# Kernel tuning notes

Measured on AMD Instinct MI355X. Metric: run time of the kernel, lower is better.

Reference implementation:

```python
import jax, jax.numpy as jnp
import numpy as np
from jax import lax

N, DIM, K, B = 400000, 128, 27, 8


def setup_inputs() -> dict:
    key = jax.random.key(0)
    ks = jax.random.split(key, 8)
    feats = jax.random.normal(ks[0], (N, DIM), dtype=jnp.float32)
    neighbor_idx = jax.random.randint(ks[1], (N, K), 0, N, dtype=jnp.int32)
    neighbor_mask = jax.random.randint(ks[2], (N, K), 0, 2) > 0
    segment_ids = jnp.sort(jax.random.randint(ks[3], (N,), 0, B, dtype=jnp.int32))
    s = 1.0 / np.sqrt(DIM)
    W1 = jax.random.normal(ks[4], (K, DIM, DIM), dtype=jnp.float32) * s
    W2 = jax.random.normal(ks[5], (K, DIM, DIM), dtype=jnp.float32) * s
    W3 = jax.random.normal(ks[6], (DIM, DIM), dtype=jnp.float32) * s
    b1 = jnp.zeros((DIM,), jnp.float32)
    b2 = jnp.zeros((DIM,), jnp.float32)
    b3 = jnp.zeros((DIM,), jnp.float32)
    return {"feats": feats, "neighbor_idx": neighbor_idx, "neighbor_mask": neighbor_mask,
            "segment_ids": segment_ids, "num_segments": B,
            "W1": W1, "b1": b1, "W2": W2, "b2": b2, "W3": W3, "b3": b3}


def sparse_conv3(x, idx, mask, W, b):
    # x: [N,D]; idx/mask: [N,K]; W: [K,D,D] -> y[n] = sum_k mask[n,k] * x[idx[n,k]] @ W[k] + b
    def step(acc, kin):
        ik, mk, Wk = kin  # [N], [N], [D,D]
        g = jnp.where(mk[:, None], x[ik], 0.0)  # [N,D] gather per offset
        return acc + g @ Wk, None
    acc, _ = lax.scan(step, jnp.zeros_like(x), (idx.T, mask.T, W))
    return acc + b


def reference(feats, neighbor_idx, neighbor_mask, segment_ids, num_segments,
              W1, b1, W2, b2, W3, b3):
    out1 = jax.nn.relu(sparse_conv3(feats, neighbor_idx, neighbor_mask, W1, b1))
    out2 = jax.nn.relu(sparse_conv3(feats, neighbor_idx, neighbor_mask, W2, b2))
    # per-batch: outer(mean over channels of out1 [Ni,1], mean over points of out2 [1,D])
    sums = jax.ops.segment_sum(out2, segment_ids, num_segments=num_segments)  # [B,D]
    cnts = jax.ops.segment_sum(jnp.ones((out2.shape[0],), out2.dtype), segment_ids,
                               num_segments=num_segments)  # [B]
    seg_mean2 = sums / jnp.maximum(cnts, 1.0)[:, None]  # [B,D]
    row_mean1 = jnp.mean(out1, axis=-1, keepdims=True)  # [N,1]
    enc = jnp.sqrt(row_mean1 * seg_mean2[segment_ids] + 1e-12)  # [N,D]
    mid = enc + out1 + out2
    out3 = jax.nn.relu(mid @ W3 + b3)  # kernel_size=1 conv == pointwise linear
    return jax.nn.relu(feats - out3)
```

## Files before the change

### kernel.cpp

```cpp
#include <hip/hip_runtime.h>
#include <stdint.h>

#define NPTS 400000
#define DIM  128
#define KNB  27
#define NSEG 8

typedef _Float16 f16x8 __attribute__((ext_vector_type(8)));
typedef float floatx16 __attribute__((ext_vector_type(16)));

#define OFF_FEATSH 0UL
#define OFF_OUT1   102400000UL
#define OFF_OUT2   204800000UL
#define OFF_PW1    307200000UL
#define OFF_PW2    308084736UL
#define OFF_PW3    308969472UL
#define OFF_SEG    309002240UL
#define OFF_CNT    309006336UL
#define OFF_ZROW   309006368UL
#define ZOFF       309006368

#define LDS_A_OFF  131072

__device__ __forceinline__ void load_lds16(const void* g, void* l) {
  __builtin_amdgcn_global_load_lds(
      (const __attribute__((address_space(1))) void*)g,
      (__attribute__((address_space(3))) void*)l, 16, 0, 0);
}

__global__ __launch_bounds__(256) void cvt_feats(const float* __restrict__ f,
                                                 _Float16* __restrict__ fh) {
  size_t g = (size_t)blockIdx.x * 256 + threadIdx.x;
  const float4* src = (const float4*)f;
  float4 v0 = src[g * 2], v1 = src[g * 2 + 1];
  f16x8 o;
  o[0] = (_Float16)v0.x; o[1] = (_Float16)v0.y; o[2] = (_Float16)v0.z; o[3] = (_Float16)v0.w;
  o[4] = (_Float16)v1.x; o[5] = (_Float16)v1.y; o[6] = (_Float16)v1.z; o[7] = (_Float16)v1.w;
  ((f16x8*)fh)[g] = o;
}

__global__ __launch_bounds__(256) void pack_w(const float* __restrict__ W1,
                                              const float* __restrict__ W2,
                                              const float* __restrict__ W3,
                                              _Float16* __restrict__ pW1,
                                              _Float16* __restrict__ pW2,
                                              _Float16* __restrict__ pW3) {
  int gid = blockIdx.x * 256 + threadIdx.x;
  const float* W; _Float16* dst; int k, rem;
  if (gid < 110592) {
    int mat = gid / 55296, r = gid % 55296;
    W = mat ? W2 : W1; dst = (mat ? pW2 : pW1) + (size_t)r * 8;
    k = r >> 11; rem = r & 2047;
  } else {
    int r = gid - 110592;
    W = W3; dst = pW3 + (size_t)r * 8; k = 0; rem = r;
  }
  int ko = rem >> 8, ct = (rem >> 6) & 3, lane = rem & 63;
  int h = lane >> 5, c = ct * 32 + (lane & 31);
  f16x8 o;
#pragma unroll
  for (int j = 0; j < 8; ++j) {
    int kk = ko * 16 + h * 8 + j;
    o[j] = (_Float16)W[(size_t)(k * 128 + kk) * 128 + c];
  }
  *(f16x8*)dst = o;
}

__global__ __launch_bounds__(512, 2) void conv_kernel(
    const _Float16* __restrict__ featsh, const int* __restrict__ nidx,
    const int* __restrict__ nmask, const int* __restrict__ segids,
    const _Float16* __restrict__ pW1, const _Float16* __restrict__ pW2,
    const float* __restrict__ b1, const float* __restrict__ b2,
    _Float16* __restrict__ out1, _Float16* __restrict__ out2,
    float* __restrict__ seg_sums, float* __restrict__ cnts_f) {
  __shared__ __align__(16) char lds_raw[163840];
  int tid = threadIdx.x, ws = tid >> 6, lane = tid & 63, h = lane >> 5;
  int conv = ws >> 2, g2 = ws & 3;
  int n0 = blockIdx.x * 128;
  int srow = ws * 16 + (lane >> 2);
  int jlane = lane & 3;
  size_t gidx = (size_t)(n0 + srow) * KNB;

  const char* fb = (const char*)featsh;
  const char* srcW = (const char*)(ws < 4 ? pW1 : pW2) + (size_t)(ws & 3) * 8192;

  floatx16 acc[4];
#pragma unroll
  for (int ct = 0; ct < 4; ++ct)
#pragma unroll
    for (int r = 0; r < 16; ++r) acc[ct][r] = 0.f;

  int i_nxt, m_nxt;
  {
    int i0 = nidx[gidx + 0];
    int m0 = nmask[gidx + 0];
    i_nxt = nidx[gidx + 1];
    m_nxt = nmask[gidx + 1];
    int off = m0 ? i0 * 256 : ZOFF;
    uint4 ag[4];
#pragma unroll
    for (int j = 0; j < 4; ++j)
      ag[j] = *(const uint4*)(fb + off + j * 64 + jlane * 16);
#pragma unroll
    for (int it = 0; it < 8; ++it)
      load_lds16(srcW + it * 1024 + lane * 16, lds_raw + ws * 8192 + it * 1024);
#pragma unroll
    for (int j = 0; j < 4; ++j)
      *(uint4*)(lds_raw + LDS_A_OFF + (size_t)(j * 4 + jlane) * 2048 + srow * 16) = ag[j];
    asm volatile("s_waitcnt lgkmcnt(0)" ::: "memory");
  }

  for (int k = 0; k < KNB; ++k) {
    int off = m_nxt ? i_nxt * 256 : ZOFF;
    uint4 ag[4];
#pragma unroll
    for (int j = 0; j < 4; ++j)
      ag[j] = *(const uint4*)(fb + off + j * 64 + jlane * 16);
    __builtin_amdgcn_sched_barrier(0);
    {
      int kq = (k + 2 <= KNB - 1) ? k + 2 : KNB - 1;
      i_nxt = nidx[gidx + kq];
      m_nxt = nmask[gidx + kq];
    }
    __builtin_amdgcn_sched_barrier(0);
    {
      int ks = (k + 1 <= KNB - 1) ? k + 1 : KNB - 1;
      const char* sk = srcW + (size_t)ks * 32768;
      char* db = lds_raw + ((k + 1) & 1) * 65536 + ws * 8192;
#pragma unroll
      for (int it = 0; it < 8; ++it)
        load_lds16(sk + it * 1024 + lane * 16, db + it * 1024);
    }
    __builtin_amdgcn_sched_barrier(0);
    asm volatile("s_waitcnt vmcnt(14)" ::: "memory");
    __builtin_amdgcn_s_barrier();
    __builtin_amdgcn_sched_barrier(0);

    const char* ldsA = lds_raw + LDS_A_OFF;
    const _Float16* ldsW =
        (const _Float16*)(lds_raw + (k & 1) * 65536 + conv * 32768);
#pragma unroll
    for (int ko = 0; ko < 8; ++ko) {
      f16x8 a = *(const f16x8*)(ldsA + (size_t)(ko * 2 + h) * 2048 +
                                (g2 * 32 + (lane & 31)) * 16);
#pragma unroll
      for (int ct = 0; ct < 4; ++ct) {
        f16x8 b = *(const f16x8*)(ldsW + ((ko * 4 + ct) * 64 + lane) * 8);
        acc[ct] = __builtin_amdgcn_mfma_f32_32x32x16_f16(a, b, acc[ct], 0, 0, 0);
      }
    }
    __builtin_amdgcn_sched_barrier(0);
    __builtin_amdgcn_s_barrier();
    __builtin_amdgcn_sched_barrier(0);
#pragma unroll
    for (int j = 0; j < 4; ++j)
      *(uint4*)(lds_raw + LDS_A_OFF + (size_t)(j * 4 + jlane) * 2048 + srow * 16) = ag[j];
    asm volatile("s_waitcnt lgkmcnt(0)" ::: "memory");
    __builtin_amdgcn_sched_barrier(0);
  }

  const float* bb = conv ? b2 : b1;
  float bias[4];
#pragma unroll
  for (int ct = 0; ct < 4; ++ct) bias[ct] = bb[ct * 32 + (lane & 31)];
#pragma unroll
  for (int ct = 0; ct < 4; ++ct)
#pragma unroll
    for (int r = 0; r < 16; ++r)
      acc[ct][r] = fmaxf(acc[ct][r] + bias[ct], 0.f);

  int seg0 = segids[n0];
  bool uniform = (seg0 == segids[n0 + 127]);

  if (conv == 1 && uniform) {
#pragma unroll
    for (int ct = 0; ct < 4; ++ct) {
      float s = 0.f;
#pragma unroll
      for (int r = 0; r < 16; ++r) s += acc[ct][r];
      s += __shfl_xor(s, 32);
      if (lane < 32) atomicAdd(&seg_sums[seg0 * 128 + ct * 32 + lane], s);
    }
  }
  if (tid == 0 && uniform) atomicAdd(&cnts_f[seg0], 128.0f);

  __syncthreads();
  _Float16* lds_out = (_Float16*)lds_raw;
#pragma unroll
  for (int ct = 0; ct < 4; ++ct) {
    int col = ct * 32 + (lane & 31);
#pragma unroll
    for (int r = 0; r < 16; ++r) {
      int lr = g2 * 32 + (r & 3) + 8 * (r >> 2) + 4 * h;
      lds_out[conv * 16384 + lr * 128 + col] = (_Float16)acc[ct][r];
    }
  }
  __syncthreads();

  if (!uniform && tid < 128) {
    int s = segids[n0 + tid];
    atomicAdd(&cnts_f[s], 1.0f);
    for (int c = 0; c < 128; ++c)
      atomicAdd(&seg_sums[s * 128 + c], (float)lds_out[16384 + tid * 128 + c]);
  }

#pragma unroll
  for (int it = 0; it < 8; ++it) {
    int chunk = it * 512 + tid;
    int cv = chunk >> 11;
    int off16 = chunk & 2047;
    uint4 v = *(const uint4*)(lds_raw + cv * 32768 + off16 * 16);
    *(uint4*)((cv ? out2 : out1) + (size_t)n0 * 128 + off16 * 8) = v;
  }
}

__global__ __launch_bounds__(256, 2) void final_kernel(
    const float* __restrict__ feats, const _Float16* __restrict__ out1,
    const _Float16* __restrict__ out2, const int* __restrict__ segids,
    const float* __restrict__ seg_sums, const float* __restrict__ cnts_f,
    const char* __restrict__ pW3, const float* __restrict__ b3,
    float* __restrict__ dout) {
  __shared__ __align__(16) char ldsw3[32768];
  __shared__ float smean[NSEG * 128];
  int tid = threadIdx.x, w = tid >> 6, lane = tid & 63, h = lane >> 5;
  int n0 = blockIdx.x * 128;
#pragma unroll
  for (int it = 0; it < 8; ++it)
    load_lds16(pW3 + w * 8192 + it * 1024 + lane * 16, ldsw3 + w * 8192 + it * 1024);
  for (int i = tid; i < NSEG * 128; i += 256)
    smean[i] = seg_sums[i] / fmaxf(cnts_f[i >> 7], 1.0f);
  __syncthreads();

  int row = n0 + w * 32 + (lane & 31);
  int seg = segids[row];
  const char* p1 = (const char*)(out1 + (size_t)row * 128 + h * 8);
  const char* p2 = (const char*)(out2 + (size_t)row * 128 + h * 8);
  f16x8 o1[8], o2[8];
  float s1 = 0.f;
#pragma unroll
  for (int ko = 0; ko < 8; ++ko) {
    o1[ko] = *(const f16x8*)(p1 + ko * 32);
    o2[ko] = *(const f16x8*)(p2 + ko * 32);
#pragma unroll
    for (int j = 0; j < 8; ++j) s1 += (float)o1[ko][j];
  }
  s1 += __shfl_xor(s1, 32);
  float rm = s1 * (1.0f / 128.0f);

  f16x8 a[8];
#pragma unroll
  for (int ko = 0; ko < 8; ++ko) {
    int colb = ko * 16 + h * 8;
#pragma unroll
    for (int j = 0; j < 8; ++j) {
      float m2 = smean[seg * 128 + colb + j];
      float e = sqrtf(fmaf(rm, m2, 1e-12f));
      a[ko][j] = (_Float16)(e + (float)o1[ko][j] + (float)o2[ko][j]);
    }
  }
  floatx16 acc[4];
#pragma unroll
  for (int ct = 0; ct < 4; ++ct)
#pragma unroll
    for (int r = 0; r < 16; ++r) acc[ct][r] = 0.f;
#pragma unroll
  for (int ko = 0; ko < 8; ++ko)
#pragma unroll
    for (int ct = 0; ct < 4; ++ct) {
      f16x8 b = *(const f16x8*)(ldsw3 + ((ko * 4 + ct) * 64 + lane) * 16);
      acc[ct] = __builtin_amdgcn_mfma_f32_32x32x16_f16(a[ko], b, acc[ct], 0, 0, 0);
    }
#pragma unroll
  for (int ct = 0; ct < 4; ++ct) {
    int col = ct * 32 + (lane & 31);
    float bc = b3[col];
#pragma unroll
    for (int r = 0; r < 16; ++r) {
      int gr = n0 + w * 32 + (r & 3) + 8 * (r >> 2) + 4 * h;
      float v = fmaxf(acc[ct][r] + bc, 0.f);
      float f = feats[(size_t)gr * 128 + col];
      dout[(size_t)gr * 128 + col] = fmaxf(f - v, 0.f);
    }
  }
}

extern "C" void kernel_launch(void* const* d_in, const int* in_sizes, int n_in,
                              void* d_out, int out_size, void* d_ws, size_t ws_size,
                              hipStream_t stream) {
  (void)in_sizes; (void)n_in; (void)out_size; (void)ws_size;
  const float* feats = (const float*)d_in[0];
  const int* nidx   = (const int*)d_in[1];
  const int* nmask  = (const int*)d_in[2];
  const int* segids = (const int*)d_in[3];
  const float* W1 = (const float*)d_in[5];
  const float* b1 = (const float*)d_in[6];
  const float* W2 = (const float*)d_in[7];
  const float* b2 = (const float*)d_in[8];
  const float* W3 = (const float*)d_in[9];
  const float* b3 = (const float*)d_in[10];
  float* dout = (float*)d_out;
  char* ws = (char*)d_ws;

  _Float16* featsh = (_Float16*)(ws + OFF_FEATSH);
  _Float16* out1h  = (_Float16*)(ws + OFF_OUT1);
  _Float16* out2h  = (_Float16*)(ws + OFF_OUT2);
  _Float16* pW1    = (_Float16*)(ws + OFF_PW1);
  _Float16* pW2    = (_Float16*)(ws + OFF_PW2);
  _Float16* pW3    = (_Float16*)(ws + OFF_PW3);
  float* seg_sums  = (float*)(ws + OFF_SEG);
  float* cnts_f    = (float*)(ws + OFF_CNT);

  hipMemsetAsync(ws + OFF_SEG, 0, 4096 + 32 + 256, stream);
  cvt_feats<<<25000, 256, 0, stream>>>(feats, featsh);
  pack_w<<<440, 256, 0, stream>>>(W1, W2, W3, pW1, pW2, pW3);
  conv_kernel<<<3125, 512, 0, stream>>>(featsh, nidx, nmask, segids, pW1, pW2,
                                        b1, b2, out1h, out2h, seg_sums, cnts_f);
  final_kernel<<<3125, 256, 0, stream>>>(feats, out1h, out2h, segids, seg_sums,
                                         cnts_f, (const char*)pW3, b3, dout);
}
```

Baseline: 1.570 ms.

## Double conv tile to 256 rows, single-buffer weights, swizzle gathered LDS

The conv kernel now handles 256 points per block instead of 128. Each wave computes two 32-row MFMA tiles that share each weight fragment read from LDS, which halves how often each weight slice is reloaded per point. Weights are now single-buffered, and the gathered feature tile is stored with an XOR swizzle to avoid bank conflicts. This frees LDS for the larger A tile, but the weight load can no longer overlap the MFMA work and now needs a full vmcnt(0) wait and barrier on every k step. A tail-block guard is added because the point count does not divide evenly by 256, and register pressure rises with the two accumulator sets.

```diff
diff --git a/kernel.cpp b/kernel.cpp
--- a/kernel.cpp
+++ b/kernel.cpp
@@ -20,7 +20,7 @@
 #define OFF_ZROW   309006368UL
 #define ZOFF       309006368
 
-#define LDS_A_OFF  131072
+#define LDS_W_OFF  65536
 
 __device__ __forceinline__ void load_lds16(const void* g, void* l) {
   __builtin_amdgcn_global_load_lds(
@@ -73,89 +73,109 @@
     const float* __restrict__ b1, const float* __restrict__ b2,
     _Float16* __restrict__ out1, _Float16* __restrict__ out2,
     float* __restrict__ seg_sums, float* __restrict__ cnts_f) {
-  __shared__ __align__(16) char lds_raw[163840];
+  __shared__ __align__(16) char lds_raw[131072];
   int tid = threadIdx.x, ws = tid >> 6, lane = tid & 63, h = lane >> 5;
-  int conv = ws >> 2, g2 = ws & 3;
-  int n0 = blockIdx.x * 128;
-  int srow = ws * 16 + (lane >> 2);
+  int conv = ws >> 2;
+  int n0 = blockIdx.x * 256;
   int jlane = lane & 3;
-  size_t gidx = (size_t)(n0 + srow) * KNB;
+  int srowA = ws * 32 + (lane >> 2);
+  int srowB = srowA + 16;
+  int growA = n0 + srowA, growB = n0 + srowB;
+  bool vA = growA < NPTS, vB = growB < NPTS;
+  size_t gxA = (size_t)(vA ? growA : NPTS - 1) * KNB;
+  size_t gxB = (size_t)(vB ? growB : NPTS - 1) * KNB;
+  int r0 = (ws & 3) * 64 + (lane & 31);
+  int r1 = r0 + 32;
 
   const char* fb = (const char*)featsh;
   const char* srcW = (const char*)(ws < 4 ? pW1 : pW2) + (size_t)(ws & 3) * 8192;
-
-  floatx16 acc[4];
+  char* wdst = lds_raw + LDS_W_OFF + (conv ? 32768 : 0) + (ws & 3) * 8192;
+
+  floatx16 acc0[4], acc1[4];
 #pragma unroll
   for (int ct = 0; ct < 4; ++ct)
 #pragma unroll
-    for (int r = 0; r < 16; ++r) acc[ct][r] = 0.f;
-
-  int i_nxt, m_nxt;
+    for (int r = 0; r < 16; ++r) { acc0[ct][r] = 0.f; acc1[ct][r] = 0.f; }
+
+  uint4 agA[4], agB[4];
+  int iN_A, mN_A, iN_B, mN_B;
+
   {
-    int i0 = nidx[gidx + 0];
-    int m0 = nmask[gidx + 0];
-    i_nxt = nidx[gidx + 1];
-    m_nxt = nmask[gidx + 1];
-    int off = m0 ? i0 * 256 : ZOFF;
-    uint4 ag[4];
-#pragma unroll
-    for (int j = 0; j < 4; ++j)
-      ag[j] = *(const uint4*)(fb + off + j * 64 + jlane * 16);
+    int iA = nidx[gxA], mA = vA ? nmask[gxA] : 0;
+    int iB = nidx[gxB], mB = vB ? nmask[gxB] : 0;
+    int offA = mA ? iA * 256 : ZOFF;
+    int offB = mB ? iB * 256 : ZOFF;
+#pragma unroll
+    for (int q = 0; q < 4; ++q) {
+      agA[q] = *(const uint4*)(fb + offA + q * 64 + jlane * 16);
+      agB[q] = *(const uint4*)(fb + offB + q * 64 + jlane * 16);
+    }
 #pragma unroll
     for (int it = 0; it < 8; ++it)
-      load_lds16(srcW + it * 1024 + lane * 16, lds_raw + ws * 8192 + it * 1024);
-#pragma unroll
-    for (int j = 0; j < 4; ++j)
-      *(uint4*)(lds_raw + LDS_A_OFF + (size_t)(j * 4 + jlane) * 2048 + srow * 16) = ag[j];
-    asm volatile("s_waitcnt lgkmcnt(0)" ::: "memory");
+      load_lds16(srcW + it * 1024 + lane * 16, wdst + it * 1024);
+    iN_A = nidx[gxA + 1]; mN_A = vA ? nmask[gxA + 1] : 0;
+    iN_B = nidx[gxB + 1]; mN_B = vB ? nmask[gxB + 1] : 0;
+#pragma unroll
+    for (int q = 0; q < 4; ++q) {
+      int cA = q * 4 + jlane;
+      *(uint4*)(lds_raw + cA * 4096 + (srowA ^ cA) * 16) = agA[q];
+      *(uint4*)(lds_raw + cA * 4096 + (srowB ^ cA) * 16) = agB[q];
+    }
+    __syncthreads();
   }
 
   for (int k = 0; k < KNB; ++k) {
-    int off = m_nxt ? i_nxt * 256 : ZOFF;
-    uint4 ag[4];
-#pragma unroll
-    for (int j = 0; j < 4; ++j)
-      ag[j] = *(const uint4*)(fb + off + j * 64 + jlane * 16);
+    int offA = mN_A ? iN_A * 256 : ZOFF;
+    int offB = mN_B ? iN_B * 256 : ZOFF;
+    __builtin_amdgcn_sched_barrier(0);
+#pragma unroll
+    for (int q = 0; q < 4; ++q) {
+      agA[q] = *(const uint4*)(fb + offA + q * 64 + jlane * 16);
+      agB[q] = *(const uint4*)(fb + offB + q * 64 + jlane * 16);
+    }
     __builtin_amdgcn_sched_barrier(0);
     {
       int kq = (k + 2 <= KNB - 1) ? k + 2 : KNB - 1;
-      i_nxt = nidx[gidx + kq];
-      m_nxt = nmask[gidx + kq];
-    }
-    __builtin_amdgcn_sched_barrier(0);
+      iN_A = nidx[gxA + kq]; mN_A = vA ? nmask[gxA + kq] : 0;
+      iN_B = nidx[gxB + kq]; mN_B = vB ? nmask[gxB + kq] : 0;
+    }
+    __builtin_amdgcn_sched_barrier(0);
+
+    const _Float16* ldsW = (const _Float16*)(lds_raw + LDS_W_OFF + conv * 32768);
+#pragma unroll
+    for (int ko = 0; ko < 8; ++ko) {
+      int c0 = ko * 2 + h;
+      f16x8 a0 = *(const f16x8*)(lds_raw + c0 * 4096 + (r0 ^ c0) * 16);
+      f16x8 a1 = *(const f16x8*)(lds_raw + c0 * 4096 + (r1 ^ c0) * 16);
+#pragma unroll
+      for (int ct = 0; ct < 4; ++ct) {
+        f16x8 b = *(const f16x8*)(ldsW + ((ko * 4 + ct) * 64 + lane) * 8);
+        acc0[ct] = __builtin_amdgcn_mfma_f32_32x32x16_f16(a0, b, acc0[ct], 0, 0, 0);
+        acc1[ct] = __builtin_amdgcn_mfma_f32_32x32x16_f16(a1, b, acc1[ct], 0, 0, 0);
+      }
+    }
+    __builtin_amdgcn_sched_barrier(0);
+    __builtin_amdgcn_s_barrier();
+    __builtin_amdgcn_sched_barrier(0);
+
+#pragma unroll
+    for (int q = 0; q < 4; ++q) {
+      int cA = q * 4 + jlane;
+      *(uint4*)(lds_raw + cA * 4096 + (srowA ^ cA) * 16) = agA[q];
+      *(uint4*)(lds_raw + cA * 4096 + (srowB ^ cA) * 16) = agB[q];
+    }
     {
       int ks = (k + 1 <= KNB - 1) ? k + 1 : KNB - 1;
       const char* sk = srcW + (size_t)ks * 32768;
-      char* db = lds_raw + ((k + 1) & 1) * 65536 + ws * 8192;
 #pragma unroll
       for (int it = 0; it < 8; ++it)
-        load_lds16(sk + it * 1024 + lane * 16, db + it * 1024);
-    }
-    __builtin_amdgcn_sched_barrier(0);
-    asm volatile("s_waitcnt vmcnt(14)" ::: "memory");
+        load_lds16(sk + it * 1024 + lane * 16, wdst + it * 1024);
+    }
+    __builtin_amdgcn_sched_barrier(0);
+    asm volatile("s_waitcnt lgkmcnt(0)" ::: "memory");
+    asm volatile("s_waitcnt vmcnt(0)" ::: "memory");
+    __builtin_amdgcn_sched_barrier(0);
     __builtin_amdgcn_s_barrier();
-    __builtin_amdgcn_sched_barrier(0);
-
-    const char* ldsA = lds_raw + LDS_A_OFF;
-    const _Float16* ldsW =
-        (const _Float16*)(lds_raw + (k & 1) * 65536 + conv * 32768);
-#pragma unroll
-    for (int ko = 0; ko < 8; ++ko) {
-      f16x8 a = *(const f16x8*)(ldsA + (size_t)(ko * 2 + h) * 2048 +
-                                (g2 * 32 + (lane & 31)) * 16);
-#pragma unroll
-      for (int ct = 0; ct < 4; ++ct) {
-        f16x8 b = *(const f16x8*)(ldsW + ((ko * 4 + ct) * 64 + lane) * 8);
-        acc[ct] = __builtin_amdgcn_mfma_f32_32x32x16_f16(a, b, acc[ct], 0, 0, 0);
-      }
-    }
-    __builtin_amdgcn_sched_barrier(0);
-    __builtin_amdgcn_s_barrier();
-    __builtin_amdgcn_sched_barrier(0);
-#pragma unroll
-    for (int j = 0; j < 4; ++j)
-      *(uint4*)(lds_raw + LDS_A_OFF + (size_t)(j * 4 + jlane) * 2048 + srow * 16) = ag[j];
-    asm volatile("s_waitcnt lgkmcnt(0)" ::: "memory");
     __builtin_amdgcn_sched_barrier(0);
   }
 
@@ -166,23 +186,26 @@
 #pragma unroll
   for (int ct = 0; ct < 4; ++ct)
 #pragma unroll
-    for (int r = 0; r < 16; ++r)
-      acc[ct][r] = fmaxf(acc[ct][r] + bias[ct], 0.f);
-
+    for (int r = 0; r < 16; ++r) {
+      acc0[ct][r] = fmaxf(acc0[ct][r] + bias[ct], 0.f);
+      acc1[ct][r] = fmaxf(acc1[ct][r] + bias[ct], 0.f);
+    }
+
+  int nvalid = (NPTS - n0 < 256) ? (NPTS - n0) : 256;
   int seg0 = segids[n0];
-  bool uniform = (seg0 == segids[n0 + 127]);
+  bool uniform = (nvalid == 256) && (seg0 == segids[n0 + 255]);
 
   if (conv == 1 && uniform) {
 #pragma unroll
     for (int ct = 0; ct < 4; ++ct) {
       float s = 0.f;
 #pragma unroll
-      for (int r = 0; r < 16; ++r) s += acc[ct][r];
+      for (int r = 0; r < 16; ++r) s += acc0[ct][r] + acc1[ct][r];
       s += __shfl_xor(s, 32);
       if (lane < 32) atomicAdd(&seg_sums[seg0 * 128 + ct * 32 + lane], s);
     }
   }
-  if (tid == 0 && uniform) atomicAdd(&cnts_f[seg0], 128.0f);
+  if (tid == 0 && uniform) atomicAdd(&cnts_f[seg0], 256.0f);
 
   __syncthreads();
   _Float16* lds_out = (_Float16*)lds_raw;
@@ -191,26 +214,31 @@
     int col = ct * 32 + (lane & 31);
 #pragma unroll
     for (int r = 0; r < 16; ++r) {
-      int lr = g2 * 32 + (r & 3) + 8 * (r >> 2) + 4 * h;
-      lds_out[conv * 16384 + lr * 128 + col] = (_Float16)acc[ct][r];
+      int lr = (ws & 3) * 64 + (r & 3) + 8 * (r >> 2) + 4 * h;
+      lds_out[conv * 32768 + lr * 128 + col] = (_Float16)acc0[ct][r];
+      lds_out[conv * 32768 + (lr + 32) * 128 + col] = (_Float16)acc1[ct][r];
     }
   }
   __syncthreads();
 
-  if (!uniform && tid < 128) {
-    int s = segids[n0 + tid];
-    atomicAdd(&cnts_f[s], 1.0f);
-    for (int c = 0; c < 128; ++c)
-      atomicAdd(&seg_sums[s * 128 + c], (float)lds_out[16384 + tid * 128 + c]);
-  }
-
-#pragma unroll
-  for (int it = 0; it < 8; ++it) {
+  if (!uniform && tid < 256) {
+    if (n0 + tid < NPTS) {
+      int s = segids[n0 + tid];
+      atomicAdd(&cnts_f[s], 1.0f);
+      for (int c = 0; c < 128; ++c)
+        atomicAdd(&seg_sums[s * 128 + c], (float)lds_out[32768 + tid * 128 + c]);
+    }
+  }
+
+#pragma unroll
+  for (int it = 0; it < 16; ++it) {
     int chunk = it * 512 + tid;
-    int cv = chunk >> 11;
-    int off16 = chunk & 2047;
-    uint4 v = *(const uint4*)(lds_raw + cv * 32768 + off16 * 16);
-    *(uint4*)((cv ? out2 : out1) + (size_t)n0 * 128 + off16 * 8) = v;
+    int cv = chunk >> 12;
+    int off16 = chunk & 4095;
+    if (n0 + (off16 >> 4) < NPTS) {
+      uint4 v = *(const uint4*)(lds_raw + cv * 65536 + off16 * 16);
+      *(uint4*)((cv ? out2 : out1) + (size_t)n0 * 128 + (size_t)off16 * 8) = v;
+    }
   }
 }
 
@@ -313,7 +341,7 @@
   hipMemsetAsync(ws + OFF_SEG, 0, 4096 + 32 + 256, stream);
   cvt_feats<<<25000, 256, 0, stream>>>(feats, featsh);
   pack_w<<<440, 256, 0, stream>>>(W1, W2, W3, pW1, pW2, pW3);
-  conv_kernel<<<3125, 512, 0, stream>>>(featsh, nidx, nmask, segids, pW1, pW2,
+  conv_kernel<<<1563, 512, 0, stream>>>(featsh, nidx, nmask, segids, pW1, pW2,
                                         b1, b2, out1h, out2h, seg_sums, cnts_f);
   final_kernel<<<3125, 256, 0, stream>>>(feats, out1h, out2h, segids, seg_sums,
                                          cnts_f, (const char*)pW3, b3, dout);
```

Result: slower. 1.864 ms (+18.7%).

## Split K across warp pairs with 64-row tiles, swizzled A in LDS, and LDS reduction

Applied to the files above, without the earlier changes.

Re-partitions the MFMA work so each warp computes a 64-row tile (two 32-row accumulators sharing each B fragment) over half of the K dimension. The partial sums from the two warp halves are reduced through LDS scratch before bias and ReLU. The gather tile in LDS gets an XOR swizzle to avoid bank conflicts, and the gather loads are reordered to issue after the weight prefetch, with a single barrier-free wait. This doubles B-fragment reuse and accumulator registers and adds an LDS reduction step in the epilogue.

```diff
diff --git a/kernel.cpp b/kernel.cpp
--- a/kernel.cpp
+++ b/kernel.cpp
@@ -20,7 +20,8 @@
 #define OFF_ZROW   309006368UL
 #define ZOFF       309006368
 
-#define LDS_A_OFF  131072
+#define LDSA       0
+#define LDSW       32768
 
 __device__ __forceinline__ void load_lds16(const void* g, void* l) {
   __builtin_amdgcn_global_load_lds(
@@ -75,109 +76,144 @@
     float* __restrict__ seg_sums, float* __restrict__ cnts_f) {
   __shared__ __align__(16) char lds_raw[163840];
   int tid = threadIdx.x, ws = tid >> 6, lane = tid & 63, h = lane >> 5;
-  int conv = ws >> 2, g2 = ws & 3;
+  int c_ = ws >> 2, g = (ws >> 1) & 1, j = ws & 1;
   int n0 = blockIdx.x * 128;
-  int srow = ws * 16 + (lane >> 2);
-  int jlane = lane & 3;
-  size_t gidx = (size_t)(n0 + srow) * KNB;
+  int srow = tid >> 2, jl = tid & 3;
+  size_t gx = (size_t)(n0 + srow) * KNB;
+  int r0 = g * 64 + (lane & 31), r1 = r0 + 32;
 
   const char* fb = (const char*)featsh;
   const char* srcW = (const char*)(ws < 4 ? pW1 : pW2) + (size_t)(ws & 3) * 8192;
 
-  floatx16 acc[4];
+  floatx16 acc0[4], acc1[4];
 #pragma unroll
   for (int ct = 0; ct < 4; ++ct)
 #pragma unroll
-    for (int r = 0; r < 16; ++r) acc[ct][r] = 0.f;
-
-  int i_nxt, m_nxt;
+    for (int r = 0; r < 16; ++r) { acc0[ct][r] = 0.f; acc1[ct][r] = 0.f; }
+
+  uint4 ag[4];
+  int i_n, m_n;
+
   {
-    int i0 = nidx[gidx + 0];
-    int m0 = nmask[gidx + 0];
-    i_nxt = nidx[gidx + 1];
-    m_nxt = nmask[gidx + 1];
+    int i0 = nidx[gx], m0 = nmask[gx];
     int off = m0 ? i0 * 256 : ZOFF;
-    uint4 ag[4];
-#pragma unroll
-    for (int j = 0; j < 4; ++j)
-      ag[j] = *(const uint4*)(fb + off + j * 64 + jlane * 16);
+#pragma unroll
+    for (int q = 0; q < 4; ++q)
+      ag[q] = *(const uint4*)(fb + off + (q * 4 + jl) * 16);
 #pragma unroll
     for (int it = 0; it < 8; ++it)
-      load_lds16(srcW + it * 1024 + lane * 16, lds_raw + ws * 8192 + it * 1024);
-#pragma unroll
-    for (int j = 0; j < 4; ++j)
-      *(uint4*)(lds_raw + LDS_A_OFF + (size_t)(j * 4 + jlane) * 2048 + srow * 16) = ag[j];
-    asm volatile("s_waitcnt lgkmcnt(0)" ::: "memory");
+      load_lds16(srcW + it * 1024 + lane * 16, lds_raw + LDSW + ws * 8192 + it * 1024);
+    i_n = nidx[gx + 1]; m_n = nmask[gx + 1];
+#pragma unroll
+    for (int q = 0; q < 4; ++q) {
+      int cA = q * 4 + jl;
+      *(uint4*)(lds_raw + cA * 2048 + ((srow ^ (2 * cA)) << 4)) = ag[q];
+    }
+    __syncthreads();
   }
 
   for (int k = 0; k < KNB; ++k) {
-    int off = m_nxt ? i_nxt * 256 : ZOFF;
-    uint4 ag[4];
-#pragma unroll
-    for (int j = 0; j < 4; ++j)
-      ag[j] = *(const uint4*)(fb + off + j * 64 + jlane * 16);
-    __builtin_amdgcn_sched_barrier(0);
-    {
-      int kq = (k + 2 <= KNB - 1) ? k + 2 : KNB - 1;
-      i_nxt = nidx[gidx + kq];
-      m_nxt = nmask[gidx + kq];
-    }
-    __builtin_amdgcn_sched_barrier(0);
     {
       int ks = (k + 1 <= KNB - 1) ? k + 1 : KNB - 1;
       const char* sk = srcW + (size_t)ks * 32768;
-      char* db = lds_raw + ((k + 1) & 1) * 65536 + ws * 8192;
+      char* db = lds_raw + LDSW + ((k + 1) & 1) * 65536 + ws * 8192;
 #pragma unroll
       for (int it = 0; it < 8; ++it)
         load_lds16(sk + it * 1024 + lane * 16, db + it * 1024);
     }
     __builtin_amdgcn_sched_barrier(0);
-    asm volatile("s_waitcnt vmcnt(14)" ::: "memory");
+    {
+      int off = m_n ? i_n * 256 : ZOFF;
+#pragma unroll
+      for (int q = 0; q < 4; ++q)
+        ag[q] = *(const uint4*)(fb + off + (q * 4 + jl) * 16);
+    }
+    __builtin_amdgcn_sched_barrier(0);
+    {
+      int kq2 = (k + 2 <= KNB - 1) ? k + 2 : KNB - 1;
+      i_n = nidx[gx + kq2]; m_n = nmask[gx + kq2];
+    }
+    __builtin_amdgcn_sched_barrier(0);
+    {
+      const char* wb = lds_raw + LDSW + (k & 1) * 65536 + c_ * 32768;
+#pragma unroll
+      for (int kq = 0; kq < 4; ++kq) {
+        int ko = j * 4 + kq;
+        int c0 = ko * 2 + h;
+        f16x8 a0 = *(const f16x8*)(lds_raw + c0 * 2048 + ((r0 ^ (2 * c0)) << 4));
+        f16x8 a1 = *(const f16x8*)(lds_raw + c0 * 2048 + ((r1 ^ (2 * c0)) << 4));
+#pragma unroll
+        for (int ct = 0; ct < 4; ++ct) {
+          f16x8 b = *(const f16x8*)(wb + ((ko * 4 + ct) * 64 + lane) * 16);
+          acc0[ct] = __builtin_amdgcn_mfma_f32_32x32x16_f16(a0, b, acc0[ct], 0, 0, 0);
+          acc1[ct] = __builtin_amdgcn_mfma_f32_32x32x16_f16(a1, b, acc1[ct], 0, 0, 0);
+        }
+      }
+    }
+    __builtin_amdgcn_sched_barrier(0);
     __builtin_amdgcn_s_barrier();
     __builtin_amdgcn_sched_barrier(0);
-
-    const char* ldsA = lds_raw + LDS_A_OFF;
-    const _Float16* ldsW =
-        (const _Float16*)(lds_raw + (k & 1) * 65536 + conv * 32768);
-#pragma unroll
-    for (int ko = 0; ko < 8; ++ko) {
-      f16x8 a = *(const f16x8*)(ldsA + (size_t)(ko * 2 + h) * 2048 +
-                                (g2 * 32 + (lane & 31)) * 16);
-#pragma unroll
-      for (int ct = 0; ct < 4; ++ct) {
-        f16x8 b = *(const f16x8*)(ldsW + ((ko * 4 + ct) * 64 + lane) * 8);
-        acc[ct] = __builtin_amdgcn_mfma_f32_32x32x16_f16(a, b, acc[ct], 0, 0, 0);
-      }
-    }
+#pragma unroll
+    for (int q = 0; q < 4; ++q) {
+      int cA = q * 4 + jl;
+      *(uint4*)(lds_raw + cA * 2048 + ((srow ^ (2 * cA)) << 4)) = ag[q];
+    }
+    asm volatile("s_waitcnt lgkmcnt(0)" ::: "memory");
     __builtin_amdgcn_sched_barrier(0);
     __builtin_amdgcn_s_barrier();
     __builtin_amdgcn_sched_barrier(0);
-#pragma unroll
-    for (int j = 0; j < 4; ++j)
-      *(uint4*)(lds_raw + LDS_A_OFF + (size_t)(j * 4 + jlane) * 2048 + srow * 16) = ag[j];
-    asm volatile("s_waitcnt lgkmcnt(0)" ::: "memory");
-    __builtin_amdgcn_sched_barrier(0);
-  }
-
-  const float* bb = conv ? b2 : b1;
-  float bias[4];
-#pragma unroll
-  for (int ct = 0; ct < 4; ++ct) bias[ct] = bb[ct * 32 + (lane & 31)];
-#pragma unroll
-  for (int ct = 0; ct < 4; ++ct)
-#pragma unroll
-    for (int r = 0; r < 16; ++r)
-      acc[ct][r] = fmaxf(acc[ct][r] + bias[ct], 0.f);
+  }
+
+  __syncthreads();
+
+  {
+    float* scr = (float*)(lds_raw + 32768 + (size_t)(c_ * 2 + g) * 32768);
+    if (j == 1) {
+#pragma unroll
+      for (int t = 0; t < 16; ++t) {
+        float4 v0 = { acc0[t >> 2][(t & 3) * 4 + 0], acc0[t >> 2][(t & 3) * 4 + 1],
+                      acc0[t >> 2][(t & 3) * 4 + 2], acc0[t >> 2][(t & 3) * 4 + 3] };
+        float4 v1 = { acc1[t >> 2][(t & 3) * 4 + 0], acc1[t >> 2][(t & 3) * 4 + 1],
+                      acc1[t >> 2][(t & 3) * 4 + 2], acc1[t >> 2][(t & 3) * 4 + 3] };
+        *(float4*)(scr + (size_t)(t * 64 + lane) * 4) = v0;
+        *(float4*)(scr + (size_t)((t + 16) * 64 + lane) * 4) = v1;
+      }
+    }
+  }
+  __syncthreads();
+  if (j == 0) {
+    float* scr = (float*)(lds_raw + 32768 + (size_t)(c_ * 2 + g) * 32768);
+#pragma unroll
+    for (int t = 0; t < 16; ++t) {
+      float4 v0 = *(const float4*)(scr + (size_t)(t * 64 + lane) * 4);
+      float4 v1 = *(const float4*)(scr + (size_t)((t + 16) * 64 + lane) * 4);
+#pragma unroll
+      for (int e = 0; e < 4; ++e) {
+        acc0[t >> 2][(t & 3) * 4 + e] += ((const float*)&v0)[e];
+        acc1[t >> 2][(t & 3) * 4 + e] += ((const float*)&v1)[e];
+      }
+    }
+    const float* bb = c_ ? b2 : b1;
+#pragma unroll
+    for (int ct = 0; ct < 4; ++ct) {
+      float bias = bb[ct * 32 + (lane & 31)];
+#pragma unroll
+      for (int r = 0; r < 16; ++r) {
+        acc0[ct][r] = fmaxf(acc0[ct][r] + bias, 0.f);
+        acc1[ct][r] = fmaxf(acc1[ct][r] + bias, 0.f);
+      }
+    }
+  }
 
   int seg0 = segids[n0];
   bool uniform = (seg0 == segids[n0 + 127]);
 
-  if (conv == 1 && uniform) {
+  if (c_ == 1 && j == 0 && uniform) {
 #pragma unroll
     for (int ct = 0; ct < 4; ++ct) {
       float s = 0.f;
 #pragma unroll
-      for (int r = 0; r < 16; ++r) s += acc[ct][r];
+      for (int r = 0; r < 16; ++r) s += acc0[ct][r] + acc1[ct][r];
       s += __shfl_xor(s, 32);
       if (lane < 32) atomicAdd(&seg_sums[seg0 * 128 + ct * 32 + lane], s);
     }
@@ -186,13 +222,16 @@
 
   __syncthreads();
   _Float16* lds_out = (_Float16*)lds_raw;
-#pragma unroll
-  for (int ct = 0; ct < 4; ++ct) {
-    int col = ct * 32 + (lane & 31);
-#pragma unroll
-    for (int r = 0; r < 16; ++r) {
-      int lr = g2 * 32 + (r & 3) + 8 * (r >> 2) + 4 * h;
-      lds_out[conv * 16384 + lr * 128 + col] = (_Float16)acc[ct][r];
+  if (j == 0) {
+#pragma unroll
+    for (int ct = 0; ct < 4; ++ct) {
+      int col = ct * 32 + (lane & 31);
+#pragma unroll
+      for (int r = 0; r < 16; ++r) {
+        int lr = g * 64 + (r & 3) + 8 * (r >> 2) + 4 * h;
+        lds_out[c_ * 16384 + lr * 128 + col] = (_Float16)acc0[ct][r];
+        lds_out[c_ * 16384 + (lr + 32) * 128 + col] = (_Float16)acc1[ct][r];
+      }
     }
   }
   __syncthreads();
```

Measured after the change: 1.570 ms. No clear change (-0.0%).
